# Kernel optimization log

Hardware: AMD Instinct MI355X
Metric: run time of the kernel (lower is better)

The kernel has to match this reference:

```python
import jax, jax.numpy as jnp
import numpy as np

B, N, C, K, OUT = 4, 16384, 64, 16, 128
BN_EPS = 1e-5


def setup_inputs() -> dict:
    key = jax.random.key(0)
    ks = jax.random.split(key, 6)
    feature = jax.random.normal(ks[0], (B, C, N), dtype=jnp.float32)
    neigh_index = jax.random.randint(ks[1], (B * N, K), 0, B * N)
    permatrix = jnp.zeros((1,), dtype=jnp.float32)  # unused by forward
    # Conv1d(in_c, in_c, kernel_size=1, bias=False) -> weight [C, C]
    W_mlp = jax.random.normal(ks[2], (C, C), dtype=jnp.float32) / np.sqrt(C).astype(np.float32)
    # Linear(in_c, out_c) -> weight [OUT, C], bias [OUT]
    W_conv = jax.random.normal(ks[3], (OUT, C), dtype=jnp.float32) / np.sqrt(C).astype(np.float32)
    b_conv = jax.random.normal(ks[4], (OUT,), dtype=jnp.float32) * 0.01
    gamma = jnp.ones((OUT,), dtype=jnp.float32)
    beta = jnp.zeros((OUT,), dtype=jnp.float32)
    return {
        "feature": feature,
        "neigh_index": neigh_index,
        "permatrix": permatrix,
        "W_mlp": W_mlp,
        "W_conv": W_conv,
        "b_conv": b_conv,
        "gamma": gamma,
        "beta": beta,
    }


def reference(feature, neigh_index, permatrix, W_mlp, W_conv, b_conv, gamma, beta):
    bsize, feats, num_pts = feature.shape
    # [B, C, N] -> [B*N, C]
    flat = feature.transpose(0, 2, 1).reshape(bsize * num_pts, feats)
    # irregular gather: [B*N, k, C]
    spirals = flat[neigh_index]
    # 1x1 conv over channels: einsum with mlp weight [C_out=C, C_in=C]
    scores = jnp.einsum("nkc,dc->nkd", spirals, W_mlp)  # [B*N, k, C]
    # softmax over channel dim (torch dim=1 on [BN, C, k] layout)
    attn = jax.nn.softmax(scores, axis=-1)
    # attention pooling over the k neighbors -> [B*N, C]
    pooled = jnp.sum(attn * spirals, axis=1)
    # Linear: [B*N, OUT]
    out = pooled @ W_conv.T + b_conv
    # [B, OUT, N]
    out = out.reshape(bsize, num_pts, -1).transpose(0, 2, 1)
    # BatchNorm1d (training-mode batch statistics) over (batch, points) per channel
    mean = jnp.mean(out, axis=(0, 2), keepdims=True)
    var = jnp.var(out, axis=(0, 2), keepdims=True)
    out = (out - mean) * jax.lax.rsqrt(var + BN_EPS)
    out = out * gamma[None, :, None] + beta[None, :, None]
    return out
```

## Files before the change

kernel.cpp:

```cpp
#include <hip/hip_runtime.h>
#include <cstdint>

#define NPTS   16384
#define BATCH  4
#define BNP    65536
#define CIN    64
#define KNB    16
#define COUT   128
#define BN_EPS 1e-5f

typedef __attribute__((ext_vector_type(8))) short     short8;
typedef __attribute__((ext_vector_type(4))) float     f32x4;
typedef __attribute__((ext_vector_type(2))) unsigned  u32x2;
typedef __attribute__((ext_vector_type(4))) int       i32x4;

__device__ __forceinline__ unsigned short f2bf(float f) {
    unsigned u = __float_as_uint(f);
    u += 0x7FFFu + ((u >> 16) & 1u);
    return (unsigned short)(u >> 16);
}
__device__ __forceinline__ float bf2f(unsigned short h) {
    return __uint_as_float(((unsigned)h) << 16);
}

__global__ __launch_bounds__(256) void k_prep(const float* __restrict__ feat,
                                              unsigned short* __restrict__ fb,
                                              const float* __restrict__ Wm,
                                              const float* __restrict__ Wc,
                                              unsigned short* __restrict__ wmb,
                                              unsigned short* __restrict__ wcb)
{
    if (blockIdx.x == 1024) {
        #pragma unroll
        for (int i = threadIdx.x; i < CIN * CIN; i += 256)       wmb[i] = f2bf(Wm[i]);
        #pragma unroll
        for (int i = threadIdx.x; i < COUT * CIN; i += 256)      wcb[i] = f2bf(Wc[i]);
        return;
    }
    __shared__ float t[CIN][CIN + 1];
    int blk = blockIdx.x;
    int b   = blk >> 8;
    int n0  = (blk & 255) << 6;
    int sub = threadIdx.x >> 6, lane = threadIdx.x & 63;
    const float* fp = feat + (size_t)b * CIN * NPTS;
    #pragma unroll
    for (int r = 0; r < CIN; r += 4) {
        int c = r + sub;
        t[c][lane] = fp[(size_t)c * NPTS + n0 + lane];
    }
    __syncthreads();
    unsigned short* ob = fb + (size_t)(b * NPTS + n0) * CIN;
    #pragma unroll
    for (int r = 0; r < CIN; r += 4) {
        int x = r + sub;
        ob[(size_t)x * CIN + lane] = f2bf(t[lane][x]);
    }
}

__global__ __launch_bounds__(256, 2) void k_main(
    const unsigned short* __restrict__ fb,
    const int* __restrict__ nidx,
    const unsigned short* __restrict__ wmb,
    const unsigned short* __restrict__ wcb,
    float* __restrict__ out)
{
    __shared__ __align__(16) unsigned short plds[4][1152];

    const int tid  = threadIdx.x;
    const int wv   = tid >> 6;
    const int lane = tid & 63;
    const int ptc  = lane & 15;
    const int qg   = lane >> 4;
    const int p4   = ptc * 4;

    short8 wmF[4][2];
    #pragma unroll
    for (int mt = 0; mt < 4; ++mt)
        #pragma unroll
        for (int ks = 0; ks < 2; ++ks)
            wmF[mt][ks] = *(const short8*)&wmb[(size_t)(mt * 16 + ptc) * CIN + qg * 8 + ks * 32];
    short8 wcF[8][2];
    #pragma unroll
    for (int mt = 0; mt < 8; ++mt)
        #pragma unroll
        for (int ks = 0; ks < 2; ++ks)
            wcF[mt][ks] = *(const short8*)&wcb[(size_t)(mt * 16 + ptc) * CIN + qg * 8 + ks * 32];

    f32x4 acc2[8];
    #pragma unroll
    for (int i = 0; i < 8; ++i) acc2[i] = (f32x4){0.f, 0.f, 0.f, 0.f};

    const int g = blockIdx.x * 4 + wv;

    i32x4 iv = *(const i32x4*)(nidx + (size_t)g * 256 + lane * 4);

    short8 rb0[4], rb1[4];
    u32x2  svr[2][4];
    int    rid[4];
    #pragma unroll
    for (int kk = 0; kk < 4; ++kk) {
        int id = __shfl(iv[kk], p4);
        rid[kk] = id;
        const unsigned short* gp = fb + (size_t)id * CIN;
        rb0[kk] = *(const short8*)(gp + qg * 8);
        rb1[kk] = *(const short8*)(gp + 32 + qg * 8);
    }
    #pragma unroll
    for (int kk = 0; kk < 2; ++kk) {
        const unsigned short* gp = fb + (size_t)rid[kk] * CIN;
        #pragma unroll
        for (int mt = 0; mt < 4; ++mt)
            svr[kk][mt] = *(const u32x2*)(gp + mt * 16 + qg * 4);
    }

    #pragma clang loop unroll(disable)
    for (int kb = 0; kb < 4; ++kb) {
        #pragma unroll
        for (int j = 0; j < 4; ++j) {
            short8 b1_0 = rb0[j];
            short8 b1_1 = rb1[j];
            f32x4 zero4 = (f32x4){0.f, 0.f, 0.f, 0.f};
            f32x4 a1[4];
            #pragma unroll
            for (int mt = 0; mt < 4; ++mt) {
                f32x4 t0 = __builtin_amdgcn_mfma_f32_16x16x32_bf16(wmF[mt][0], b1_0, zero4, 0, 0, 0);
                a1[mt]   = __builtin_amdgcn_mfma_f32_16x16x32_bf16(wmF[mt][1], b1_1, t0,    0, 0, 0);
            }

            if (kb != 3) {
                int id = __shfl(iv[j], p4 + kb + 1);
                rid[j] = id;
                const unsigned short* gp = fb + (size_t)id * CIN;
                rb0[j] = *(const short8*)(gp + qg * 8);
                rb1[j] = *(const short8*)(gp + 32 + qg * 8);
            }

            float s = 0.f;
            #pragma unroll
            for (int mt = 0; mt < 4; ++mt)
                #pragma unroll
                for (int r = 0; r < 4; ++r) {
                    float x = __expf(a1[mt][r]);
                    a1[mt][r] = x;
                    s += x;
                }
            s += __shfl_xor(s, 16);
            s += __shfl_xor(s, 32);
            float inv = __builtin_amdgcn_rcpf(s);

            unsigned short* pl = plds[wv];
            #pragma unroll
            for (int mt = 0; mt < 4; ++mt) {
                u32x2 sv = svr[j & 1][mt];
                unsigned lo = sv[0], hi = sv[1];
                float p0 = bf2f((unsigned short)lo)         * (a1[mt][0] * inv);
                float p1 = bf2f((unsigned short)(lo >> 16)) * (a1[mt][1] * inv);
                float p2 = bf2f((unsigned short)hi)         * (a1[mt][2] * inv);
                float p3 = bf2f((unsigned short)(hi >> 16)) * (a1[mt][3] * inv);
                unsigned w0 = ((__float_as_uint(p0) + 0x8000u) >> 16) |
                              ((__float_as_uint(p1) + 0x8000u) & 0xFFFF0000u);
                unsigned w1 = ((__float_as_uint(p2) + 0x8000u) >> 16) |
                              ((__float_as_uint(p3) + 0x8000u) & 0xFFFF0000u);
                *(u32x2*)&pl[ptc * 72 + mt * 16 + qg * 4] = (u32x2){w0, w1};
            }

            if (j < 2 || kb != 3) {
                const unsigned short* gp = fb + (size_t)rid[(j + 2) & 3] * CIN;
                #pragma unroll
                for (int mt = 0; mt < 4; ++mt)
                    svr[j & 1][mt] = *(const u32x2*)(gp + mt * 16 + qg * 4);
            }

            short8 b2_0 = *(const short8*)&pl[ptc * 72 +      qg * 8];
            short8 b2_1 = *(const short8*)&pl[ptc * 72 + 32 + qg * 8];

            #pragma unroll
            for (int mt = 0; mt < 8; ++mt) {
                acc2[mt] = __builtin_amdgcn_mfma_f32_16x16x32_bf16(wcF[mt][0], b2_0, acc2[mt], 0, 0, 0);
                acc2[mt] = __builtin_amdgcn_mfma_f32_16x16x32_bf16(wcF[mt][1], b2_1, acc2[mt], 0, 0, 0);
            }
        }
    }

    {
        int p0 = g * KNB;
        int b  = p0 >> 14;
        int nn = (p0 & (NPTS - 1)) + ptc;
        float* ob = out + (((size_t)b * COUT) << 14) + nn;
        #pragma unroll
        for (int mt = 0; mt < 8; ++mt)
            #pragma unroll
            for (int r = 0; r < 4; ++r)
                ob[((size_t)(mt * 16 + qg * 4 + r)) << 14] = acc2[mt][r];
    }
}

__global__ __launch_bounds__(256) void k_part(const float* __restrict__ out,
                                              float* __restrict__ part)
{
    int o = blockIdx.x >> 2, b = blockIdx.x & 3;
    const float4* p = (const float4*)(out + (((size_t)(b * COUT + o)) << 14));
    float s = 0.f, q = 0.f;
    for (int i = threadIdx.x; i < NPTS / 4; i += 256) {
        float4 v = p[i];
        s += (v.x + v.y) + (v.z + v.w);
        q += (v.x * v.x + v.y * v.y) + (v.z * v.z + v.w * v.w);
    }
    #pragma unroll
    for (int off = 32; off >= 1; off >>= 1) {
        s += __shfl_xor(s, off);
        q += __shfl_xor(q, off);
    }
    __shared__ float ls[4], lq[4];
    if ((threadIdx.x & 63) == 0) { ls[threadIdx.x >> 6] = s; lq[threadIdx.x >> 6] = q; }
    __syncthreads();
    if (threadIdx.x == 0) {
        part[blockIdx.x * 2]     = (ls[0] + ls[1]) + (ls[2] + ls[3]);
        part[blockIdx.x * 2 + 1] = (lq[0] + lq[1]) + (lq[2] + lq[3]);
    }
}

__global__ __launch_bounds__(256) void k_apply(float* __restrict__ out,
                                               const float* __restrict__ part,
                                               const float* __restrict__ gamma,
                                               const float* __restrict__ beta)
{
    __shared__ float sc[COUT], sh[COUT];
    int t = threadIdx.x;
    if (t < COUT) {
        float s = 0.f, q = 0.f;
        #pragma unroll
        for (int j = 0; j < 4; ++j) {
            s += part[(t * 4 + j) * 2];
            q += part[(t * 4 + j) * 2 + 1];
        }
        float mean = s * (1.0f / BNP);
        float var  = q * (1.0f / BNP) - mean * mean;
        float a = gamma[t] * rsqrtf(var + BN_EPS);
        sc[t] = a; sh[t] = beta[t] - mean * a;
    }
    __syncthreads();
    const int total4 = BATCH * COUT * NPTS / 4;
    for (long i = (long)blockIdx.x * 256 + t; i < total4; i += (long)gridDim.x * 256) {
        int ch = ((int)(i >> 12)) & 127;
        float4 v = ((float4*)out)[i];
        float a = sc[ch], b2 = sh[ch];
        v.x = fmaf(v.x, a, b2); v.y = fmaf(v.y, a, b2);
        v.z = fmaf(v.z, a, b2); v.w = fmaf(v.w, a, b2);
        ((float4*)out)[i] = v;
    }
}

extern "C" void kernel_launch(void* const* d_in, const int* in_sizes, int n_in,
                              void* d_out, int out_size, void* d_ws, size_t ws_size,
                              hipStream_t stream)
{
    const float* feat  = (const float*)d_in[0];
    const int*   nidx  = (const int*)  d_in[1];
    const float* Wm    = (const float*)d_in[3];
    const float* Wc    = (const float*)d_in[4];
    const float* gamma = (const float*)d_in[6];
    const float* beta  = (const float*)d_in[7];
    float* out = (float*)d_out;

    char* ws = (char*)d_ws;
    unsigned short* fb   = (unsigned short*)ws;
    float*          part = (float*)(ws + (size_t)BNP * CIN * 2);
    unsigned short* wmb  = (unsigned short*)(ws + (size_t)BNP * CIN * 2 + 4096);
    unsigned short* wcb  = wmb + CIN * CIN;

    k_prep <<<1025, 256, 0, stream>>>(feat, fb, Wm, Wc, wmb, wcb);
    k_main <<<1024, 256, 0, stream>>>(fb, nidx, wmb, wcb, out);
    k_part <<<512,  256, 0, stream>>>(out, part);
    k_apply<<<2048, 256, 0, stream>>>(out, part, gamma, beta);
}
```

Before: 166.8 us.

## Process two neighbor slots per step with double-buffered LDS, fully unrolled loop

```diff
diff --git a/kernel.cpp b/kernel.cpp
--- a/kernel.cpp
+++ b/kernel.cpp
@@ -64,7 +64,7 @@
     const unsigned short* __restrict__ wcb,
     float* __restrict__ out)
 {
-    __shared__ __align__(16) unsigned short plds[4][1152];
+    __shared__ __align__(16) unsigned short plds[4][2][1152];
 
     const int tid  = threadIdx.x;
     const int wv   = tid >> 6;
@@ -95,7 +95,7 @@
     i32x4 iv = *(const i32x4*)(nidx + (size_t)g * 256 + lane * 4);
 
     short8 rb0[4], rb1[4];
-    u32x2  svr[2][4];
+    u32x2  svr[4][4];
     int    rid[4];
     #pragma unroll
     for (int kk = 0; kk < 4; ++kk) {
@@ -104,81 +104,108 @@
         const unsigned short* gp = fb + (size_t)id * CIN;
         rb0[kk] = *(const short8*)(gp + qg * 8);
         rb1[kk] = *(const short8*)(gp + 32 + qg * 8);
-    }
-    #pragma unroll
-    for (int kk = 0; kk < 2; ++kk) {
-        const unsigned short* gp = fb + (size_t)rid[kk] * CIN;
         #pragma unroll
         for (int mt = 0; mt < 4; ++mt)
             svr[kk][mt] = *(const u32x2*)(gp + mt * 16 + qg * 4);
     }
 
-    #pragma clang loop unroll(disable)
-    for (int kb = 0; kb < 4; ++kb) {
-        #pragma unroll
-        for (int j = 0; j < 4; ++j) {
-            short8 b1_0 = rb0[j];
-            short8 b1_1 = rb1[j];
-            f32x4 zero4 = (f32x4){0.f, 0.f, 0.f, 0.f};
-            f32x4 a1[4];
+    #pragma unroll
+    for (int p = 0; p < 8; ++p) {
+        const int sA = (2 * p) & 3;
+        const int sB = sA + 1;
+
+        f32x4 zero4 = (f32x4){0.f, 0.f, 0.f, 0.f};
+        f32x4 a1A[4], a1B[4];
+        #pragma unroll
+        for (int mt = 0; mt < 4; ++mt) {
+            f32x4 t0 = __builtin_amdgcn_mfma_f32_16x16x32_bf16(wmF[mt][0], rb0[sA], zero4, 0, 0, 0);
+            a1A[mt]  = __builtin_amdgcn_mfma_f32_16x16x32_bf16(wmF[mt][1], rb1[sA], t0,    0, 0, 0);
+        }
+        #pragma unroll
+        for (int mt = 0; mt < 4; ++mt) {
+            f32x4 t0 = __builtin_amdgcn_mfma_f32_16x16x32_bf16(wmF[mt][0], rb0[sB], zero4, 0, 0, 0);
+            a1B[mt]  = __builtin_amdgcn_mfma_f32_16x16x32_bf16(wmF[mt][1], rb1[sB], t0,    0, 0, 0);
+        }
+
+        if (p < 6) {
+            int idA = __shfl(iv[sA], p4 + ((2 * p + 4) >> 2));
+            int idB = __shfl(iv[sB], p4 + ((2 * p + 5) >> 2));
+            rid[sA] = idA;
+            rid[sB] = idB;
+            const unsigned short* gA = fb + (size_t)idA * CIN;
+            const unsigned short* gB = fb + (size_t)idB * CIN;
+            rb0[sA] = *(const short8*)(gA + qg * 8);
+            rb1[sA] = *(const short8*)(gA + 32 + qg * 8);
+            rb0[sB] = *(const short8*)(gB + qg * 8);
+            rb1[sB] = *(const short8*)(gB + 32 + qg * 8);
+        }
+
+        float ssA = 0.f, ssB = 0.f;
+        #pragma unroll
+        for (int mt = 0; mt < 4; ++mt)
+            #pragma unroll
+            for (int r = 0; r < 4; ++r) {
+                float xA = __expf(a1A[mt][r]);
+                float xB = __expf(a1B[mt][r]);
+                a1A[mt][r] = xA;  ssA += xA;
+                a1B[mt][r] = xB;  ssB += xB;
+            }
+        ssA += __shfl_xor(ssA, 16);
+        ssB += __shfl_xor(ssB, 16);
+        ssA += __shfl_xor(ssA, 32);
+        ssB += __shfl_xor(ssB, 32);
+        float invA = __builtin_amdgcn_rcpf(ssA);
+        float invB = __builtin_amdgcn_rcpf(ssB);
+
+        #pragma unroll
+        for (int mt = 0; mt < 4; ++mt) {
+            u32x2 svA = svr[sA][mt], svB = svr[sB][mt];
+            unsigned loA = svA[0], hiA = svA[1];
+            unsigned loB = svB[0], hiB = svB[1];
+            float pA0 = bf2f((unsigned short)loA)         * (a1A[mt][0] * invA);
+            float pA1 = bf2f((unsigned short)(loA >> 16)) * (a1A[mt][1] * invA);
+            float pA2 = bf2f((unsigned short)hiA)         * (a1A[mt][2] * invA);
+            float pA3 = bf2f((unsigned short)(hiA >> 16)) * (a1A[mt][3] * invA);
+            float pB0 = bf2f((unsigned short)loB)         * (a1B[mt][0] * invB);
+            float pB1 = bf2f((unsigned short)(loB >> 16)) * (a1B[mt][1] * invB);
+            float pB2 = bf2f((unsigned short)hiB)         * (a1B[mt][2] * invB);
+            float pB3 = bf2f((unsigned short)(hiB >> 16)) * (a1B[mt][3] * invB);
+            unsigned wA0 = ((__float_as_uint(pA0) + 0x8000u) >> 16) |
+                           ((__float_as_uint(pA1) + 0x8000u) & 0xFFFF0000u);
+            unsigned wA1 = ((__float_as_uint(pA2) + 0x8000u) >> 16) |
+                           ((__float_as_uint(pA3) + 0x8000u) & 0xFFFF0000u);
+            unsigned wB0 = ((__float_as_uint(pB0) + 0x8000u) >> 16) |
+                           ((__float_as_uint(pB1) + 0x8000u) & 0xFFFF0000u);
+            unsigned wB1 = ((__float_as_uint(pB2) + 0x8000u) >> 16) |
+                           ((__float_as_uint(pB3) + 0x8000u) & 0xFFFF0000u);
+            *(u32x2*)&plds[wv][0][ptc * 72 + mt * 16 + qg * 4] = (u32x2){wA0, wA1};
+            *(u32x2*)&plds[wv][1][ptc * 72 + mt * 16 + qg * 4] = (u32x2){wB0, wB1};
+        }
+
+        if (p < 6) {
+            const unsigned short* gA = fb + (size_t)rid[sA] * CIN;
+            const unsigned short* gB = fb + (size_t)rid[sB] * CIN;
             #pragma unroll
             for (int mt = 0; mt < 4; ++mt) {
-                f32x4 t0 = __builtin_amdgcn_mfma_f32_16x16x32_bf16(wmF[mt][0], b1_0, zero4, 0, 0, 0);
-                a1[mt]   = __builtin_amdgcn_mfma_f32_16x16x32_bf16(wmF[mt][1], b1_1, t0,    0, 0, 0);
+                svr[sA][mt] = *(const u32x2*)(gA + mt * 16 + qg * 4);
+                svr[sB][mt] = *(const u32x2*)(gB + mt * 16 + qg * 4);
             }
-
-            if (kb != 3) {
-                int id = __shfl(iv[j], p4 + kb + 1);
-                rid[j] = id;
-                const unsigned short* gp = fb + (size_t)id * CIN;
-                rb0[j] = *(const short8*)(gp + qg * 8);
-                rb1[j] = *(const short8*)(gp + 32 + qg * 8);
-            }
-
-            float s = 0.f;
-            #pragma unroll
-            for (int mt = 0; mt < 4; ++mt)
-                #pragma unroll
-                for (int r = 0; r < 4; ++r) {
-                    float x = __expf(a1[mt][r]);
-                    a1[mt][r] = x;
-                    s += x;
-                }
-            s += __shfl_xor(s, 16);
-            s += __shfl_xor(s, 32);
-            float inv = __builtin_amdgcn_rcpf(s);
-
-            unsigned short* pl = plds[wv];
-            #pragma unroll
-            for (int mt = 0; mt < 4; ++mt) {
-                u32x2 sv = svr[j & 1][mt];
-                unsigned lo = sv[0], hi = sv[1];
-                float p0 = bf2f((unsigned short)lo)         * (a1[mt][0] * inv);
-                float p1 = bf2f((unsigned short)(lo >> 16)) * (a1[mt][1] * inv);
-                float p2 = bf2f((unsigned short)hi)         * (a1[mt][2] * inv);
-                float p3 = bf2f((unsigned short)(hi >> 16)) * (a1[mt][3] * inv);
-                unsigned w0 = ((__float_as_uint(p0) + 0x8000u) >> 16) |
-                              ((__float_as_uint(p1) + 0x8000u) & 0xFFFF0000u);
-                unsigned w1 = ((__float_as_uint(p2) + 0x8000u) >> 16) |
-                              ((__float_as_uint(p3) + 0x8000u) & 0xFFFF0000u);
-                *(u32x2*)&pl[ptc * 72 + mt * 16 + qg * 4] = (u32x2){w0, w1};
-            }
-
-            if (j < 2 || kb != 3) {
-                const unsigned short* gp = fb + (size_t)rid[(j + 2) & 3] * CIN;
-                #pragma unroll
-                for (int mt = 0; mt < 4; ++mt)
-                    svr[j & 1][mt] = *(const u32x2*)(gp + mt * 16 + qg * 4);
-            }
-
-            short8 b2_0 = *(const short8*)&pl[ptc * 72 +      qg * 8];
-            short8 b2_1 = *(const short8*)&pl[ptc * 72 + 32 + qg * 8];
-
-            #pragma unroll
-            for (int mt = 0; mt < 8; ++mt) {
-                acc2[mt] = __builtin_amdgcn_mfma_f32_16x16x32_bf16(wcF[mt][0], b2_0, acc2[mt], 0, 0, 0);
-                acc2[mt] = __builtin_amdgcn_mfma_f32_16x16x32_bf16(wcF[mt][1], b2_1, acc2[mt], 0, 0, 0);
-            }
+        }
+
+        short8 b2A0 = *(const short8*)&plds[wv][0][ptc * 72 +      qg * 8];
+        short8 b2A1 = *(const short8*)&plds[wv][0][ptc * 72 + 32 + qg * 8];
+        short8 b2B0 = *(const short8*)&plds[wv][1][ptc * 72 +      qg * 8];
+        short8 b2B1 = *(const short8*)&plds[wv][1][ptc * 72 + 32 + qg * 8];
+
+        #pragma unroll
+        for (int mt = 0; mt < 8; ++mt) {
+            acc2[mt] = __builtin_amdgcn_mfma_f32_16x16x32_bf16(wcF[mt][0], b2A0, acc2[mt], 0, 0, 0);
+            acc2[mt] = __builtin_amdgcn_mfma_f32_16x16x32_bf16(wcF[mt][1], b2A1, acc2[mt], 0, 0, 0);
+        }
+        #pragma unroll
+        for (int mt = 0; mt < 8; ++mt) {
+            acc2[mt] = __builtin_amdgcn_mfma_f32_16x16x32_bf16(wcF[mt][0], b2B0, acc2[mt], 0, 0, 0);
+            acc2[mt] = __builtin_amdgcn_mfma_f32_16x16x32_bf16(wcF[mt][1], b2B1, acc2[mt], 0, 0, 0);
         }
     }
 
```

New measurement: 165.5 us. Within noise of the previous version (-0.8%).
